# Performance work log

Measured on AMD Instinct MI355X. Metric: run time of the kernel, lower is better.

The kernel has to match this reference:

```python
import jax, jax.numpy as jnp
import numpy as np

# Equal-time-constant (tau_mem == tau_syn) closed-form spike time, as in
# fastAndDeep utils_spiketime_et: for each causal set of the k earliest input
# spikes, t = tau * (b/a - W0(-c/a * exp(b/a))), with
#   a = sum_k w_k exp(t_k/tau),  b = sum_k w_k t_k exp(t_k/tau) / tau,
#   c = (threshold - leak) * g_leak.
TAU = 1.0
THRESHOLD = 1.0
LEAK = 0.0
G_LEAK = 1.0
INV_E = float(np.exp(-1.0))


def lambertw0(z):
    """Principal-branch Lambert W for z in [-1/e, 0), via Halley iterations."""
    z = jnp.clip(z, -INV_E + 1e-8, -1e-30)
    # branch-point expansion near -1/e, series z(1-z) elsewhere
    w = jnp.where(z < -0.2,
                  -1.0 + jnp.sqrt(2.0 * (1.0 + jnp.e * z)),
                  z * (1.0 - z))
    for _ in range(12):
        ew = jnp.exp(w)
        f = w * ew - z
        wp1 = w + 1.0
        w = w - f / (ew * wp1 - (w + 2.0) * f / (2.0 * wp1))
    return w


def setup_inputs() -> dict:
    key = jax.random.key(0)
    k1, k2 = jax.random.split(key)
    B, NPRE, NPOST = 128, 1024, 256
    # spike times in units of tau, all finite
    input_spikes = jax.random.uniform(k1, (B, NPRE), dtype=jnp.float32)
    # positive weights scaled so many neurons cross threshold
    input_weights = jax.random.uniform(k2, (NPRE, NPOST), dtype=jnp.float32) * 0.1
    return {"input_spikes": input_spikes, "input_weights": input_weights}


def reference(input_spikes, input_weights):
    # input_spikes: (B, NPRE), input_weights: (NPRE, NPOST)
    sort_idx = jnp.argsort(input_spikes, axis=1)                       # (B, NPRE)
    sorted_spikes = jnp.take_along_axis(input_spikes, sort_idx, axis=1)
    sorted_w = input_weights[sort_idx]                                 # (B, NPRE, NPOST)

    inf_mask = jnp.isinf(sorted_spikes)
    s = jnp.where(inf_mask, 0.0, sorted_spikes)[..., None]             # (B, NPRE, 1)
    sw = jnp.where(inf_mask[..., None], 0.0, sorted_w)

    e = jnp.exp(s / TAU)
    a = jnp.cumsum(sw * e, axis=1)                                     # (B, NPRE, NPOST)
    b = jnp.cumsum(sw * s * e, axis=1) / TAU
    c = (THRESHOLD - LEAK) * G_LEAK

    a_safe = jnp.where(jnp.abs(a) > 1e-10, a, 1e-10)
    z = -c / a_safe * jnp.exp(jnp.clip(b / a_safe, -30.0, 30.0))
    valid = (a > 0) & (z >= -INV_E)
    t = TAU * (b / a_safe - lambertw0(z))
    t = jnp.where(valid, t, jnp.inf)                                   # candidate spike times

    # causal-set consistency: spike must be after the k-th sorted input and
    # not later than the (k+1)-th sorted input (last row exempt)
    ss = sorted_spikes[..., None]
    not_after_last = t < ss
    next_spike = jnp.roll(sorted_spikes, -1, axis=1)[..., None]
    not_earlier_than_next = (t > next_spike).at[:, -1, :].set(False)
    t = jnp.where(not_after_last | not_earlier_than_next, jnp.inf, t)

    output_spikes = jnp.min(t, axis=1)                                 # (B, NPOST)
    return output_spikes
```

## Files before the change

### kernel.cpp

```cpp
#include <hip/hip_runtime.h>
#include <math.h>

#define BATCH 128
#define NPRE  1024
#define NPOST 256
#define NJB   128
#define NW    16
#define KPW   8
#define CLEN  128
#define NCHK  8

__device__ __forceinline__ float lambertw0_f(float z) {
    const float INV_E = 0.36787944117144233f;
    float zc = fminf(fmaxf(z, -INV_E + 1e-8f), -1e-30f);
    float w;
    if (zc < -0.2f) {
        w = -1.0f + sqrtf(2.0f * (1.0f + 2.718281828459045f * zc));
    } else {
        w = zc * (1.0f - zc);
    }
#pragma unroll
    for (int it = 0; it < 12; ++it) {
        float ew  = expf(w);
        float f   = w * ew - zc;
        float wp1 = w + 1.0f;
        w = w - f / (ew * wp1 - (w + 2.0f) * f / (2.0f * wp1));
    }
    return w;
}

__global__ __launch_bounds__(1024, 4)
void ttfs_kernel(const float* __restrict__ spikes,
                 const float* __restrict__ Wt,
                 float* __restrict__ out)
{
    __shared__ int    cnt[1024];
    __shared__ int    bstart[1025];
    __shared__ int    wsum[NW];
    __shared__ unsigned long long tmp64[NPRE];
    __shared__ float4 tab[NPRE + 1];
    __shared__ int    sidx[NPRE + 4];
    __shared__ float  pA[NW][NJB + 2], pB[NW][NJB + 2];
    __shared__ int    flags[2];

    const int tid  = threadIdx.x;
    const int lane = tid & 63;
    const int wid  = tid >> 6;
    const int b    = (int)blockIdx.x >> 1;
    const int h    = (int)blockIdx.x & 1;

    {
        float s = spikes[b * NPRE + tid];
        unsigned long long v =
            (((unsigned long long)__float_as_uint(s)) << 32) | (unsigned)tid;
        int bucket = (int)(s * 1024.0f);
        bucket = bucket < 0 ? 0 : (bucket > 1023 ? 1023 : bucket);

        cnt[tid] = 0;
        __syncthreads();
        int arr = atomicAdd(&cnt[bucket], 1);
        __syncthreads();

        int c0 = cnt[tid];
        int x  = c0;
#pragma unroll
        for (int d = 1; d < 64; d <<= 1) {
            int y = __shfl_up(x, d);
            if (lane >= d) x += y;
        }
        if (lane == 63) wsum[wid] = x;
        __syncthreads();
        int base = 0;
        for (int w = 0; w < wid; ++w) base += wsum[w];
        bstart[tid] = base + x - c0;
        if (tid == 0) bstart[1024] = NPRE;
        __syncthreads();

        int slot = bstart[bucket] + arr;
        tmp64[slot] = v;
        __syncthreads();

        int st = bstart[bucket], en = bstart[bucket + 1];
        int rk = 0;
        for (int q = st; q < en; ++q) rk += (tmp64[q] < v);
        int fin = st + rk;

        float e = expf(s);
        tab[fin]  = make_float4(s, e, s * e, 0.0f);
        sidx[fin] = tid;
    }
    if (tid == 0) {
        tab[NPRE]  = make_float4(INFINITY, INFINITY, 0.0f, 0.0f);
        sidx[NPRE] = 0; sidx[NPRE + 1] = 0; sidx[NPRE + 2] = 0; sidx[NPRE + 3] = 0;
    }
    __syncthreads();

    const int j0 = h * NJB;
    const float* __restrict__ Wc0 = Wt + j0 + lane;
    const float* __restrict__ Wc1 = Wt + j0 + 64 + lane;
    const int4* __restrict__ sidx4 = (const int4*)sidx;
    const int kbase = wid * KPW;

    float offA = 0.0f, offB = 0.0f;
    float preA = 0.0f, preB = 0.0f;
    int   baseK = -1;
    bool  doneJ = false;

#define LOADW2(kstart, dst)                                                   \
    {                                                                         \
        int4 Ia = sidx4[(kstart) >> 2];                                       \
        int4 Ib = sidx4[((kstart) + 4) >> 2];                                 \
        dst[0]  = Wc0[Ia.x * NPOST]; dst[1]  = Wc0[Ia.y * NPOST];             \
        dst[2]  = Wc0[Ia.z * NPOST]; dst[3]  = Wc0[Ia.w * NPOST];             \
        dst[4]  = Wc0[Ib.x * NPOST]; dst[5]  = Wc0[Ib.y * NPOST];             \
        dst[6]  = Wc0[Ib.z * NPOST]; dst[7]  = Wc0[Ib.w * NPOST];             \
        dst[8]  = Wc1[Ia.x * NPOST]; dst[9]  = Wc1[Ia.y * NPOST];             \
        dst[10] = Wc1[Ia.z * NPOST]; dst[11] = Wc1[Ia.w * NPOST];             \
        dst[12] = Wc1[Ib.x * NPOST]; dst[13] = Wc1[Ib.y * NPOST];             \
        dst[14] = Wc1[Ib.z * NPOST]; dst[15] = Wc1[Ib.w * NPOST];             \
    }

    float wv[2 * KPW], wn[2 * KPW];
    LOADW2(kbase, wv);

    for (int ch = 0; ch < NCHK; ++ch) {
        const int kk0 = ch * CLEN + kbase;
        if (ch < NCHK - 1) LOADW2(kk0 + CLEN, wn);
        float a0 = 0.0f, b0 = 0.0f, a1 = 0.0f, b1 = 0.0f;
#pragma unroll
        for (int i = 0; i < KPW; ++i) {
            float4 t = tab[kk0 + i];
            a0 = fmaf(wv[i],       t.y, a0);
            b0 = fmaf(wv[i],       t.z, b0);
            a1 = fmaf(wv[KPW + i], t.y, a1);
            b1 = fmaf(wv[KPW + i], t.z, b1);
        }
        pA[wid][lane]      = a0; pB[wid][lane]      = b0;
        pA[wid][64 + lane] = a1; pB[wid][64 + lane] = b1;
        __syncthreads();

        if (wid < 2) {
            const int n = (wid << 6) + lane;
#pragma unroll
            for (int w = 0; w < NW; ++w) {
                float nA = offA + pA[w][n];
                float nB = offB + pB[w][n];
                if (!doneJ) {
                    float4 tn = tab[ch * CLEN + (w + 1) * KPW];
                    float gate = fmaf(nA, tn.x, -nB);
                    if (gate >= tn.y) {
                        baseK = ch * CLEN + w * KPW;
                        preA = offA; preB = offB;
                        doneJ = true;
                    }
                }
                offA = nA; offB = nB;
            }
            bool all = __all(doneJ);
            if (lane == 0) flags[wid] = all ? 1 : 0;
        }
        __syncthreads();
        if (flags[0] & flags[1]) break;
        if (ch < NCHK - 1) {
#pragma unroll
            for (int i = 0; i < 2 * KPW; ++i) wv[i] = wn[i];
        }
    }

    if (wid < 2) {
        const int n = (wid << 6) + lane;
        const float* __restrict__ Wcol = Wt + j0 + n;
        float result = INFINITY;
        const float INV_E = 0.36787944117144233f;
        if (doneJ) {
            float wl[KPW];
#pragma unroll
            for (int i = 0; i < KPW; ++i) wl[i] = Wcol[sidx[baseK + i] * NPOST];
            float A = preA, Bq = preB;
            int fk = -1; float fA = 0.0f, fB = 0.0f;
#pragma unroll
            for (int i = 0; i < KPW; ++i) {
                const int k = baseK + i;
                float4 t = tab[k];
                A  = fmaf(wl[i], t.y, A);
                Bq = fmaf(wl[i], t.z, Bq);
                if (fk < 0) {
                    float4 tn = tab[k + 1];
                    float gate = fmaf(A, tn.x, -Bq);
                    if (gate >= tn.y) { fA = A; fB = Bq; fk = k; }
                }
            }

            if (fk >= 0) {
                float r  = fB / fA;
                float ez = expf(fminf(fmaxf(r, -30.0f), 30.0f));
                float z  = -ez / fA;
                bool valid = (fA > 0.0f) && (z >= -INV_E);
                float t = r - lambertw0_f(z);
                bool ok = valid && (t >= tab[fk].x) && (fk == NPRE - 1 || t <= tab[fk + 1].x);
                if (ok) {
                    result = t;
                } else {
                    float A2 = fA, B2 = fB;
                    for (int k = fk + 1; k < NPRE; ++k) {
                        float w = Wcol[sidx[k] * NPOST];
                        float4 t3 = tab[k];
                        A2 = fmaf(w, t3.y, A2);
                        B2 = fmaf(w, t3.z, B2);
                        if (A2 <= 0.0f) continue;
                        float r2  = B2 / A2;
                        float ez2 = expf(fminf(fmaxf(r2, -30.0f), 30.0f));
                        float z2  = -ez2 / A2;
                        if (z2 < -INV_E) continue;
                        float t2 = r2 - lambertw0_f(z2);
                        if (t2 < t3.x) continue;
                        if (k < NPRE - 1 && t2 > tab[k + 1].x) continue;
                        result = t2;
                        break;
                    }
                }
            } else {
                float A2 = 0.0f, B2 = 0.0f;
                for (int k = 0; k < NPRE; ++k) {
                    float w = Wcol[sidx[k] * NPOST];
                    float4 t3 = tab[k];
                    A2 = fmaf(w, t3.y, A2);
                    B2 = fmaf(w, t3.z, B2);
                    if (A2 <= 0.0f) continue;
                    float r2  = B2 / A2;
                    float ez2 = expf(fminf(fmaxf(r2, -30.0f), 30.0f));
                    float z2  = -ez2 / A2;
                    if (z2 < -INV_E) continue;
                    float t2 = r2 - lambertw0_f(z2);
                    if (t2 < t3.x) continue;
                    if (k < NPRE - 1 && t2 > tab[k + 1].x) continue;
                    result = t2;
                    break;
                }
            }
        }
        out[b * NPOST + j0 + n] = result;
    }
}

extern "C" void kernel_launch(void* const* d_in, const int* in_sizes, int n_in,
                              void* d_out, int out_size, void* d_ws, size_t ws_size,
                              hipStream_t stream) {
    const float* spikes  = (const float*)d_in[0];
    const float* weights = (const float*)d_in[1];
    float* outp = (float*)d_out;
    ttfs_kernel<<<dim3(BATCH * 2), dim3(1024), 0, stream>>>(spikes, weights, outp);
}
```

Baseline: 15.21 us.

## Split each batch row across four blocks of 64 output neurons

Each block now handles 64 post-synaptic columns instead of 128, so the grid grows from 256 to 512 blocks. Each thread loads half as many weights per chunk, and the scan and finalisation run on a single wave. The float4 table is split into two float2 tables so that LDS reads fetch only the fields needed. The trade-off is that the per-row sort and exp preprocessing is now repeated in four blocks instead of two, and the launch-bounds occupancy hint is raised.

New measurement: 15.81 us. +3.9%, slower.

```diff
diff --git a/kernel.cpp b/kernel.cpp
--- a/kernel.cpp
+++ b/kernel.cpp
@@ -4,7 +4,7 @@
 #define BATCH 128
 #define NPRE  1024
 #define NPOST 256
-#define NJB   128
+#define NJB   64
 #define NW    16
 #define KPW   8
 #define CLEN  128
@@ -29,7 +29,7 @@
     return w;
 }
 
-__global__ __launch_bounds__(1024, 4)
+__global__ __launch_bounds__(1024, 8)
 void ttfs_kernel(const float* __restrict__ spikes,
                  const float* __restrict__ Wt,
                  float* __restrict__ out)
@@ -38,16 +38,17 @@
     __shared__ int    bstart[1025];
     __shared__ int    wsum[NW];
     __shared__ unsigned long long tmp64[NPRE];
-    __shared__ float4 tab[NPRE + 1];
+    __shared__ float2 tse[NPRE + 1];
+    __shared__ float2 tez[NPRE + 1];
     __shared__ int    sidx[NPRE + 4];
-    __shared__ float  pA[NW][NJB + 2], pB[NW][NJB + 2];
-    __shared__ int    flags[2];
+    __shared__ float  pA[NW][NJB + 1], pB[NW][NJB + 1];
+    __shared__ int    allDoneFlag;
 
     const int tid  = threadIdx.x;
     const int lane = tid & 63;
     const int wid  = tid >> 6;
-    const int b    = (int)blockIdx.x >> 1;
-    const int h    = (int)blockIdx.x & 1;
+    const int b    = (int)blockIdx.x >> 2;
+    const int h    = (int)blockIdx.x & 3;
 
     {
         float s = spikes[b * NPRE + tid];
@@ -86,18 +87,19 @@
         int fin = st + rk;
 
         float e = expf(s);
-        tab[fin]  = make_float4(s, e, s * e, 0.0f);
+        tse[fin]  = make_float2(s, e);
+        tez[fin]  = make_float2(e, s * e);
         sidx[fin] = tid;
     }
     if (tid == 0) {
-        tab[NPRE]  = make_float4(INFINITY, INFINITY, 0.0f, 0.0f);
+        tse[NPRE]  = make_float2(INFINITY, INFINITY);
+        tez[NPRE]  = make_float2(INFINITY, 0.0f);
         sidx[NPRE] = 0; sidx[NPRE + 1] = 0; sidx[NPRE + 2] = 0; sidx[NPRE + 3] = 0;
     }
     __syncthreads();
 
     const int j0 = h * NJB;
-    const float* __restrict__ Wc0 = Wt + j0 + lane;
-    const float* __restrict__ Wc1 = Wt + j0 + 64 + lane;
+    const float* __restrict__ Wcol = Wt + j0 + lane;
     const int4* __restrict__ sidx4 = (const int4*)sidx;
     const int kbase = wid * KPW;
 
@@ -106,47 +108,39 @@
     int   baseK = -1;
     bool  doneJ = false;
 
-#define LOADW2(kstart, dst)                                                   \
+#define LOADW(kstart, dst)                                                    \
     {                                                                         \
         int4 Ia = sidx4[(kstart) >> 2];                                       \
         int4 Ib = sidx4[((kstart) + 4) >> 2];                                 \
-        dst[0]  = Wc0[Ia.x * NPOST]; dst[1]  = Wc0[Ia.y * NPOST];             \
-        dst[2]  = Wc0[Ia.z * NPOST]; dst[3]  = Wc0[Ia.w * NPOST];             \
-        dst[4]  = Wc0[Ib.x * NPOST]; dst[5]  = Wc0[Ib.y * NPOST];             \
-        dst[6]  = Wc0[Ib.z * NPOST]; dst[7]  = Wc0[Ib.w * NPOST];             \
-        dst[8]  = Wc1[Ia.x * NPOST]; dst[9]  = Wc1[Ia.y * NPOST];             \
-        dst[10] = Wc1[Ia.z * NPOST]; dst[11] = Wc1[Ia.w * NPOST];             \
-        dst[12] = Wc1[Ib.x * NPOST]; dst[13] = Wc1[Ib.y * NPOST];             \
-        dst[14] = Wc1[Ib.z * NPOST]; dst[15] = Wc1[Ib.w * NPOST];             \
-    }
-
-    float wv[2 * KPW], wn[2 * KPW];
-    LOADW2(kbase, wv);
+        dst[0] = Wcol[Ia.x * NPOST]; dst[1] = Wcol[Ia.y * NPOST];             \
+        dst[2] = Wcol[Ia.z * NPOST]; dst[3] = Wcol[Ia.w * NPOST];             \
+        dst[4] = Wcol[Ib.x * NPOST]; dst[5] = Wcol[Ib.y * NPOST];             \
+        dst[6] = Wcol[Ib.z * NPOST]; dst[7] = Wcol[Ib.w * NPOST];             \
+    }
+
+    float wv[KPW], wn[KPW];
+    LOADW(kbase, wv);
 
     for (int ch = 0; ch < NCHK; ++ch) {
         const int kk0 = ch * CLEN + kbase;
-        if (ch < NCHK - 1) LOADW2(kk0 + CLEN, wn);
-        float a0 = 0.0f, b0 = 0.0f, a1 = 0.0f, b1 = 0.0f;
+        if (ch < NCHK - 1) LOADW(kk0 + CLEN, wn);
+        float a0 = 0.0f, b0 = 0.0f;
 #pragma unroll
         for (int i = 0; i < KPW; ++i) {
-            float4 t = tab[kk0 + i];
-            a0 = fmaf(wv[i],       t.y, a0);
-            b0 = fmaf(wv[i],       t.z, b0);
-            a1 = fmaf(wv[KPW + i], t.y, a1);
-            b1 = fmaf(wv[KPW + i], t.z, b1);
-        }
-        pA[wid][lane]      = a0; pB[wid][lane]      = b0;
-        pA[wid][64 + lane] = a1; pB[wid][64 + lane] = b1;
-        __syncthreads();
-
-        if (wid < 2) {
-            const int n = (wid << 6) + lane;
+            float2 t = tez[kk0 + i];
+            a0 = fmaf(wv[i], t.x, a0);
+            b0 = fmaf(wv[i], t.y, b0);
+        }
+        pA[wid][lane] = a0; pB[wid][lane] = b0;
+        __syncthreads();
+
+        if (wid == 0) {
 #pragma unroll
             for (int w = 0; w < NW; ++w) {
-                float nA = offA + pA[w][n];
-                float nB = offB + pB[w][n];
+                float nA = offA + pA[w][lane];
+                float nB = offB + pB[w][lane];
                 if (!doneJ) {
-                    float4 tn = tab[ch * CLEN + (w + 1) * KPW];
+                    float2 tn = tse[ch * CLEN + (w + 1) * KPW];
                     float gate = fmaf(nA, tn.x, -nB);
                     if (gate >= tn.y) {
                         baseK = ch * CLEN + w * KPW;
@@ -157,19 +151,17 @@
                 offA = nA; offB = nB;
             }
             bool all = __all(doneJ);
-            if (lane == 0) flags[wid] = all ? 1 : 0;
-        }
-        __syncthreads();
-        if (flags[0] & flags[1]) break;
+            if (lane == 0) allDoneFlag = all ? 1 : 0;
+        }
+        __syncthreads();
+        if (allDoneFlag) break;
         if (ch < NCHK - 1) {
 #pragma unroll
-            for (int i = 0; i < 2 * KPW; ++i) wv[i] = wn[i];
-        }
-    }
-
-    if (wid < 2) {
-        const int n = (wid << 6) + lane;
-        const float* __restrict__ Wcol = Wt + j0 + n;
+            for (int i = 0; i < KPW; ++i) wv[i] = wn[i];
+        }
+    }
+
+    if (wid == 0) {
         float result = INFINITY;
         const float INV_E = 0.36787944117144233f;
         if (doneJ) {
@@ -181,11 +173,11 @@
 #pragma unroll
             for (int i = 0; i < KPW; ++i) {
                 const int k = baseK + i;
-                float4 t = tab[k];
-                A  = fmaf(wl[i], t.y, A);
-                Bq = fmaf(wl[i], t.z, Bq);
+                float2 ez = tez[k];
+                A  = fmaf(wl[i], ez.x, A);
+                Bq = fmaf(wl[i], ez.y, Bq);
                 if (fk < 0) {
-                    float4 tn = tab[k + 1];
+                    float2 tn = tse[k + 1];
                     float gate = fmaf(A, tn.x, -Bq);
                     if (gate >= tn.y) { fA = A; fB = Bq; fk = k; }
                 }
@@ -193,28 +185,29 @@
 
             if (fk >= 0) {
                 float r  = fB / fA;
-                float ez = expf(fminf(fmaxf(r, -30.0f), 30.0f));
-                float z  = -ez / fA;
+                float ezz = expf(fminf(fmaxf(r, -30.0f), 30.0f));
+                float z  = -ezz / fA;
                 bool valid = (fA > 0.0f) && (z >= -INV_E);
                 float t = r - lambertw0_f(z);
-                bool ok = valid && (t >= tab[fk].x) && (fk == NPRE - 1 || t <= tab[fk + 1].x);
+                bool ok = valid && (t >= tse[fk].x) &&
+                          (fk == NPRE - 1 || t <= tse[fk + 1].x);
                 if (ok) {
                     result = t;
                 } else {
                     float A2 = fA, B2 = fB;
                     for (int k = fk + 1; k < NPRE; ++k) {
                         float w = Wcol[sidx[k] * NPOST];
-                        float4 t3 = tab[k];
-                        A2 = fmaf(w, t3.y, A2);
-                        B2 = fmaf(w, t3.z, B2);
+                        float2 ez2v = tez[k];
+                        A2 = fmaf(w, ez2v.x, A2);
+                        B2 = fmaf(w, ez2v.y, B2);
                         if (A2 <= 0.0f) continue;
                         float r2  = B2 / A2;
-                        float ez2 = expf(fminf(fmaxf(r2, -30.0f), 30.0f));
-                        float z2  = -ez2 / A2;
+                        float ex2 = expf(fminf(fmaxf(r2, -30.0f), 30.0f));
+                        float z2  = -ex2 / A2;
                         if (z2 < -INV_E) continue;
                         float t2 = r2 - lambertw0_f(z2);
-                        if (t2 < t3.x) continue;
-                        if (k < NPRE - 1 && t2 > tab[k + 1].x) continue;
+                        if (t2 < tse[k].x) continue;
+                        if (k < NPRE - 1 && t2 > tse[k + 1].x) continue;
                         result = t2;
                         break;
                     }
@@ -223,23 +216,23 @@
                 float A2 = 0.0f, B2 = 0.0f;
                 for (int k = 0; k < NPRE; ++k) {
                     float w = Wcol[sidx[k] * NPOST];
-                    float4 t3 = tab[k];
-                    A2 = fmaf(w, t3.y, A2);
-                    B2 = fmaf(w, t3.z, B2);
+                    float2 ez2v = tez[k];
+                    A2 = fmaf(w, ez2v.x, A2);
+                    B2 = fmaf(w, ez2v.y, B2);
                     if (A2 <= 0.0f) continue;
                     float r2  = B2 / A2;
-                    float ez2 = expf(fminf(fmaxf(r2, -30.0f), 30.0f));
-                    float z2  = -ez2 / A2;
+                    float ex2 = expf(fminf(fmaxf(r2, -30.0f), 30.0f));
+                    float z2  = -ex2 / A2;
                     if (z2 < -INV_E) continue;
                     float t2 = r2 - lambertw0_f(z2);
-                    if (t2 < t3.x) continue;
-                    if (k < NPRE - 1 && t2 > tab[k + 1].x) continue;
+                    if (t2 < tse[k].x) continue;
+                    if (k < NPRE - 1 && t2 > tse[k + 1].x) continue;
                     result = t2;
                     break;
                 }
             }
         }
-        out[b * NPOST + j0 + n] = result;
+        out[b * NPOST + j0 + lane] = result;
     }
 }
 
@@ -249,5 +242,5 @@
     const float* spikes  = (const float*)d_in[0];
     const float* weights = (const float*)d_in[1];
     float* outp = (float*)d_out;
-    ttfs_kernel<<<dim3(BATCH * 2), dim3(1024), 0, stream>>>(spikes, weights, outp);
+    ttfs_kernel<<<dim3(BATCH * 4), dim3(1024), 0, stream>>>(spikes, weights, outp);
 }
```
